# Performance work log

Hardware: AMD Instinct MI355X
Metric: run time of the kernel (lower is better)

## Reference

```python
import jax, jax.numpy as jnp
import numpy as np

P = 128        # num proposals
C_ALL = 19     # instance_classes + 1
C = 18         # instance classes used in the loop
M = 400000     # total (proposal, point) membership entries
N_PTS = 65536  # num points
SCORE_THR = 0.001
MASK_THR = -0.5
NPOINT_THR = 100


def setup_inputs() -> dict:
    key = jax.random.key(0)
    k1, k2, k3, k4, k5 = jax.random.split(key, 5)
    return {
        "cls_scores": jax.random.normal(k1, (P, C_ALL), dtype=jnp.float32),
        "scores": jax.random.normal(k2, (P, C_ALL), dtype=jnp.float32),
        "mask_scores": jax.random.normal(k3, (M, C_ALL), dtype=jnp.float32),
        "prop_ids": jax.random.randint(k4, (M,), 0, P, dtype=jnp.int32),
        "point_ids": jax.random.randint(k5, (M,), 0, N_PTS, dtype=jnp.int32),
        "num_points": N_PTS,
    }


def reference(cls_scores, scores, mask_scores, prop_ids, point_ids, num_points):
    # cls_scores, scores: [P, C+1]; mask_scores: [M, C+1]
    # prop_ids/point_ids: [M] -> membership of point in proposal
    n_prop = cls_scores.shape[0]
    cls_soft = jax.nn.softmax(cls_scores, axis=1)              # [P, C+1]
    # scores_pred_i = clamp(scores[:, i], 0, 1) * cls_soft[:, i], for each class i
    scores_pred = (jnp.clip(scores[:, :C], 0.0, 1.0) * cls_soft[:, :C]).T  # [C, P]

    # per-class mask threshold then scatter 1s into dense [P, N] proposal masks
    mask_keep = (mask_scores[:, :C] > MASK_THR).astype(jnp.int32).T        # [C, M]

    def scatter_one_class(m):
        # duplicates resolved with max (matches repeated assignment of 1)
        return jnp.zeros((n_prop, num_points), jnp.int32).at[prop_ids, point_ids].max(m)

    dense = jax.vmap(scatter_one_class)(mask_keep)             # [C, P, N] int32

    pointnum = dense.sum(axis=-1)                              # [C, P]
    keep = (cls_soft[:, :C].T > SCORE_THR) \
        & (scores_pred > -1.0) \
        & (pointnum >= NPOINT_THR)                             # [C, P]

    proposals_pred = dense * keep[..., None].astype(jnp.int32)  # zero invalid rows
    cluster_scores = jnp.where(keep, scores_pred, 0.0)
    semantic_id = jnp.broadcast_to((jnp.arange(C) + 1)[:, None], (C, n_prop))
    return proposals_pred, cluster_scores, keep, semantic_id
```

## Files before the change

### kernel.cpp

```cpp
#include <hip/hip_runtime.h>
#include <stdint.h>

#define NPROP   128
#define C_ALL   19
#define NCLS    18
#define M_TOTAL 400000
#define NPTS    65536
#define CP      (NCLS * NPROP)
#define PTS_PER_CHUNK 8192
#define NCHUNK  (NPTS / PTS_PER_CHUNK)

struct WS {
    float        spred[CP];
    unsigned int keepA[CP];
    unsigned int pointnum[CP];
    unsigned int dense[(size_t)NPROP * NPTS];
};

__global__ void zero_kernel(WS* ws) {
    const size_t tid = (size_t)blockIdx.x * blockDim.x + threadIdx.x;
    const size_t stride = (size_t)gridDim.x * blockDim.x;
    uint4* d4 = (uint4*)ws->dense;
    const size_t n4 = (size_t)NPROP * NPTS / 4;
    const uint4 z = make_uint4(0u, 0u, 0u, 0u);
    for (size_t j = tid; j < n4; j += stride) d4[j] = z;
    if (tid < CP) ws->pointnum[tid] = 0;
}

__global__ void prep_kernel(const float* __restrict__ cls_scores,
                            const float* __restrict__ scores,
                            WS* ws) {
    int p = threadIdx.x;
    if (p >= NPROP) return;
    float row[C_ALL];
    float mx = -3.4e38f;
    #pragma unroll
    for (int i = 0; i < C_ALL; ++i) {
        row[i] = cls_scores[p * C_ALL + i];
        mx = fmaxf(mx, row[i]);
    }
    float s = 0.0f;
    #pragma unroll
    for (int i = 0; i < C_ALL; ++i) {
        row[i] = __expf(row[i] - mx);
        s += row[i];
    }
    float inv = 1.0f / s;
    #pragma unroll
    for (int c = 0; c < NCLS; ++c) {
        float soft = row[c] * inv;
        float sc = scores[p * C_ALL + c];
        sc = fminf(fmaxf(sc, 0.0f), 1.0f);
        float sp = sc * soft;
        ws->spred[c * NPROP + p] = sp;
        ws->keepA[c * NPROP + p] = (soft > 0.001f && sp > -1.0f) ? 1u : 0u;
    }
}

__global__ void scatter_kernel(const float* __restrict__ mask_scores,
                               const int* __restrict__ prop_ids,
                               const int* __restrict__ point_ids,
                               WS* ws) {
    int m = blockIdx.x * blockDim.x + threadIdx.x;
    if (m >= M_TOTAL) return;
    const float* r = mask_scores + (size_t)m * C_ALL;
    unsigned int bits = 0;
    #pragma unroll
    for (int c = 0; c < NCLS; ++c)
        bits |= (unsigned int)(r[c] > -0.5f) << c;
    const size_t addr = ((size_t)prop_ids[m] << 16) | (unsigned int)point_ids[m];
    atomicOr(&ws->dense[addr], bits);
}

__global__ __launch_bounds__(256) void count_kernel(WS* ws) {
    __shared__ unsigned int cnt[NCLS];
    const int p = blockIdx.x;
    const int chunk = blockIdx.y;
    const int t = threadIdx.x;
    if (t < NCLS) cnt[t] = 0;
    __syncthreads();

    const unsigned int* base = ws->dense + ((size_t)p << 16) + chunk * (NPTS / 4);
    unsigned int local[NCLS] = {0};
    for (int i = t; i < NPTS / 4; i += 256) {
        unsigned int w = base[i];
        #pragma unroll
        for (int c = 0; c < NCLS; ++c) local[c] += (w >> c) & 1u;
    }
    #pragma unroll
    for (int c = 0; c < NCLS; ++c) {
        unsigned int v = local[c];
        #pragma unroll
        for (int off = 32; off > 0; off >>= 1) v += __shfl_down(v, off, 64);
        if ((t & 63) == 0) atomicAdd(&cnt[c], v);
    }
    __syncthreads();
    if (t < NCLS) atomicAdd(&ws->pointnum[t * NPROP + p], cnt[t]);
}

__global__ __launch_bounds__(256) void write_kernel(const WS* __restrict__ ws,
                                                    float* __restrict__ out) {
    __shared__ unsigned int lds[PTS_PER_CHUNK];
    __shared__ float sk[NCLS];
    const int p = blockIdx.x;
    const int chunk = blockIdx.y;
    const int t = threadIdx.x;

    const uint4* src4 = (const uint4*)(ws->dense + ((size_t)p << 16) + chunk * PTS_PER_CHUNK);
    uint4* lds4 = (uint4*)lds;
    #pragma unroll
    for (int j = 0; j < (PTS_PER_CHUNK / 4) / 256; ++j)
        lds4[j * 256 + t] = src4[j * 256 + t];

    if (t < NCLS) {
        const int cp = t * NPROP + p;
        const bool k = (ws->keepA[cp] != 0u) && (ws->pointnum[cp] >= 100u);
        sk[t] = k ? 1.0f : 0.0f;
        if (chunk == 0) {
            float* outCS = out + (size_t)CP * NPTS;
            float* outK  = outCS + CP;
            float* outS  = outK  + CP;
            outCS[cp] = k ? ws->spred[cp] : 0.0f;
            outK[cp]  = k ? 1.0f : 0.0f;
            outS[cp]  = (float)(t + 1);
        }
    }
    __syncthreads();

    const float4 z = make_float4(0.f, 0.f, 0.f, 0.f);
    #pragma unroll 1
    for (int c = 0; c < NCLS; ++c) {
        float4* dst = (float4*)(out + (((size_t)(c * NPROP + p)) << 16)) +
                      chunk * (PTS_PER_CHUNK / 4);
        if (sk[c] != 0.0f) {
            #pragma unroll
            for (int j = 0; j < (PTS_PER_CHUNK / 4) / 256; ++j) {
                const int idx = j * 256 + t;
                uint4 w = lds4[idx];
                float4 v;
                v.x = (w.x >> c) & 1u ? 1.0f : 0.0f;
                v.y = (w.y >> c) & 1u ? 1.0f : 0.0f;
                v.z = (w.z >> c) & 1u ? 1.0f : 0.0f;
                v.w = (w.w >> c) & 1u ? 1.0f : 0.0f;
                dst[idx] = v;
            }
        } else {
            #pragma unroll
            for (int j = 0; j < (PTS_PER_CHUNK / 4) / 256; ++j)
                dst[j * 256 + t] = z;
        }
    }
}

extern "C" void kernel_launch(void* const* d_in, const int* in_sizes, int n_in,
                              void* d_out, int out_size, void* d_ws, size_t ws_size,
                              hipStream_t stream) {
    const float* cls_scores  = (const float*)d_in[0];
    const float* scores      = (const float*)d_in[1];
    const float* mask_scores = (const float*)d_in[2];
    const int*   prop_ids    = (const int*)d_in[3];
    const int*   point_ids   = (const int*)d_in[4];

    WS* ws = (WS*)d_ws;
    float* out = (float*)d_out;

    zero_kernel<<<2048, 256, 0, stream>>>(ws);
    prep_kernel<<<1, NPROP, 0, stream>>>(cls_scores, scores, ws);

    const int blocksM = (M_TOTAL + 255) / 256;
    scatter_kernel<<<blocksM, 256, 0, stream>>>(mask_scores, prop_ids, point_ids, ws);

    count_kernel<<<dim3(NPROP, 4), 256, 0, stream>>>(ws);
    write_kernel<<<dim3(NPROP, NCHUNK), 256, 0, stream>>>(ws, out);
}
```

Baseline: 172.3 us.

## Fuse zero/prep kernels, vectorize count loads, nontemporal branchless output writes

Merges the workspace zeroing and softmax prep into one launch, removing one kernel launch. The count kernel now reads uint4 words with a fully unrolled loop. The write kernel swaps grid order so the chunk index is the fast dimension, replaces the keep branch with a multiply-select by the keep flag, and uses nontemporal stores for the large float output. The aim is lower launch overhead and better streaming-store throughput on the output, which is about 600 MB. The cost is that rows that are not kept now read LDS and do the bit tests too.

```diff
diff --git a/kernel.cpp b/kernel.cpp
--- a/kernel.cpp
+++ b/kernel.cpp
@@ -8,7 +8,9 @@
 #define NPTS    65536
 #define CP      (NCLS * NPROP)
 #define PTS_PER_CHUNK 8192
-#define NCHUNK  (NPTS / PTS_PER_CHUNK)
+#define NCHUNK  8
+
+typedef float f32x4 __attribute__((ext_vector_type(4)));
 
 struct WS {
     float        spred[CP];
@@ -17,7 +19,8 @@
     unsigned int dense[(size_t)NPROP * NPTS];
 };
 
-__global__ void zero_kernel(WS* ws) {
+__global__ void zero_prep_kernel(const float* __restrict__ cls_scores,
+                                 const float* __restrict__ scores, WS* ws) {
     const size_t tid = (size_t)blockIdx.x * blockDim.x + threadIdx.x;
     const size_t stride = (size_t)gridDim.x * blockDim.x;
     uint4* d4 = (uint4*)ws->dense;
@@ -25,35 +28,31 @@
     const uint4 z = make_uint4(0u, 0u, 0u, 0u);
     for (size_t j = tid; j < n4; j += stride) d4[j] = z;
     if (tid < CP) ws->pointnum[tid] = 0;
-}
-
-__global__ void prep_kernel(const float* __restrict__ cls_scores,
-                            const float* __restrict__ scores,
-                            WS* ws) {
-    int p = threadIdx.x;
-    if (p >= NPROP) return;
-    float row[C_ALL];
-    float mx = -3.4e38f;
-    #pragma unroll
-    for (int i = 0; i < C_ALL; ++i) {
-        row[i] = cls_scores[p * C_ALL + i];
-        mx = fmaxf(mx, row[i]);
-    }
-    float s = 0.0f;
-    #pragma unroll
-    for (int i = 0; i < C_ALL; ++i) {
-        row[i] = __expf(row[i] - mx);
-        s += row[i];
-    }
-    float inv = 1.0f / s;
-    #pragma unroll
-    for (int c = 0; c < NCLS; ++c) {
-        float soft = row[c] * inv;
-        float sc = scores[p * C_ALL + c];
-        sc = fminf(fmaxf(sc, 0.0f), 1.0f);
-        float sp = sc * soft;
-        ws->spred[c * NPROP + p] = sp;
-        ws->keepA[c * NPROP + p] = (soft > 0.001f && sp > -1.0f) ? 1u : 0u;
+    if (tid < NPROP) {
+        const int p = (int)tid;
+        float row[C_ALL];
+        float mx = -3.4e38f;
+        #pragma unroll
+        for (int i = 0; i < C_ALL; ++i) {
+            row[i] = cls_scores[p * C_ALL + i];
+            mx = fmaxf(mx, row[i]);
+        }
+        float s = 0.0f;
+        #pragma unroll
+        for (int i = 0; i < C_ALL; ++i) {
+            row[i] = __expf(row[i] - mx);
+            s += row[i];
+        }
+        const float inv = 1.0f / s;
+        #pragma unroll
+        for (int c = 0; c < NCLS; ++c) {
+            const float soft = row[c] * inv;
+            float sc = scores[p * C_ALL + c];
+            sc = fminf(fmaxf(sc, 0.0f), 1.0f);
+            const float sp = sc * soft;
+            ws->spred[c * NPROP + p] = sp;
+            ws->keepA[c * NPROP + p] = (soft > 0.001f && sp > -1.0f) ? 1u : 0u;
+        }
     }
 }
 
@@ -75,23 +74,28 @@
 __global__ __launch_bounds__(256) void count_kernel(WS* ws) {
     __shared__ unsigned int cnt[NCLS];
     const int p = blockIdx.x;
-    const int chunk = blockIdx.y;
+    const int quarter = blockIdx.y;
     const int t = threadIdx.x;
     if (t < NCLS) cnt[t] = 0;
     __syncthreads();
-
-    const unsigned int* base = ws->dense + ((size_t)p << 16) + chunk * (NPTS / 4);
-    unsigned int local[NCLS] = {0};
-    for (int i = t; i < NPTS / 4; i += 256) {
-        unsigned int w = base[i];
+    const uint4* base4 = (const uint4*)(ws->dense + ((size_t)p << 16) +
+                                        quarter * (NPTS / 4));
+    unsigned int local[NCLS];
+    #pragma unroll
+    for (int c = 0; c < NCLS; ++c) local[c] = 0;
+    #pragma unroll
+    for (int j = 0; j < (NPTS / 16) / 256; ++j) {
+        const uint4 w = base4[j * 256 + t];
         #pragma unroll
-        for (int c = 0; c < NCLS; ++c) local[c] += (w >> c) & 1u;
+        for (int c = 0; c < NCLS; ++c)
+            local[c] += ((w.x >> c) & 1u) + ((w.y >> c) & 1u) +
+                        ((w.z >> c) & 1u) + ((w.w >> c) & 1u);
     }
     #pragma unroll
     for (int c = 0; c < NCLS; ++c) {
         unsigned int v = local[c];
         #pragma unroll
-        for (int off = 32; off > 0; off >>= 1) v += __shfl_down(v, off, 64);
+        for (int off = 32; off; off >>= 1) v += __shfl_down(v, off, 64);
         if ((t & 63) == 0) atomicAdd(&cnt[c], v);
     }
     __syncthreads();
@@ -102,11 +106,12 @@
                                                     float* __restrict__ out) {
     __shared__ unsigned int lds[PTS_PER_CHUNK];
     __shared__ float sk[NCLS];
-    const int p = blockIdx.x;
-    const int chunk = blockIdx.y;
-    const int t = threadIdx.x;
+    const int chunk = blockIdx.x;
+    const int p     = blockIdx.y;
+    const int t     = threadIdx.x;
 
-    const uint4* src4 = (const uint4*)(ws->dense + ((size_t)p << 16) + chunk * PTS_PER_CHUNK);
+    const uint4* src4 = (const uint4*)(ws->dense + ((size_t)p << 16) +
+                                       chunk * PTS_PER_CHUNK);
     uint4* lds4 = (uint4*)lds;
     #pragma unroll
     for (int j = 0; j < (PTS_PER_CHUNK / 4) / 256; ++j)
@@ -127,27 +132,21 @@
     }
     __syncthreads();
 
-    const float4 z = make_float4(0.f, 0.f, 0.f, 0.f);
     #pragma unroll 1
     for (int c = 0; c < NCLS; ++c) {
-        float4* dst = (float4*)(out + (((size_t)(c * NPROP + p)) << 16)) +
-                      chunk * (PTS_PER_CHUNK / 4);
-        if (sk[c] != 0.0f) {
-            #pragma unroll
-            for (int j = 0; j < (PTS_PER_CHUNK / 4) / 256; ++j) {
-                const int idx = j * 256 + t;
-                uint4 w = lds4[idx];
-                float4 v;
-                v.x = (w.x >> c) & 1u ? 1.0f : 0.0f;
-                v.y = (w.y >> c) & 1u ? 1.0f : 0.0f;
-                v.z = (w.z >> c) & 1u ? 1.0f : 0.0f;
-                v.w = (w.w >> c) & 1u ? 1.0f : 0.0f;
-                dst[idx] = v;
-            }
-        } else {
-            #pragma unroll
-            for (int j = 0; j < (PTS_PER_CHUNK / 4) / 256; ++j)
-                dst[j * 256 + t] = z;
+        const float kf = sk[c];
+        f32x4* dst = (f32x4*)(out + (((size_t)(c * NPROP + p)) << 16)) +
+                     chunk * (PTS_PER_CHUNK / 4);
+        #pragma unroll
+        for (int j = 0; j < (PTS_PER_CHUNK / 4) / 256; ++j) {
+            const int idx = j * 256 + t;
+            const uint4 w = lds4[idx];
+            f32x4 v;
+            v.x = ((w.x >> c) & 1u) ? kf : 0.0f;
+            v.y = ((w.y >> c) & 1u) ? kf : 0.0f;
+            v.z = ((w.z >> c) & 1u) ? kf : 0.0f;
+            v.w = ((w.w >> c) & 1u) ? kf : 0.0f;
+            __builtin_nontemporal_store(v, &dst[idx]);
         }
     }
 }
@@ -164,12 +163,9 @@
     WS* ws = (WS*)d_ws;
     float* out = (float*)d_out;
 
-    zero_kernel<<<2048, 256, 0, stream>>>(ws);
-    prep_kernel<<<1, NPROP, 0, stream>>>(cls_scores, scores, ws);
-
+    zero_prep_kernel<<<2048, 256, 0, stream>>>(cls_scores, scores, ws);
     const int blocksM = (M_TOTAL + 255) / 256;
     scatter_kernel<<<blocksM, 256, 0, stream>>>(mask_scores, prop_ids, point_ids, ws);
-
     count_kernel<<<dim3(NPROP, 4), 256, 0, stream>>>(ws);
-    write_kernel<<<dim3(NPROP, NCHUNK), 256, 0, stream>>>(ws, out);
+    write_kernel<<<dim3(NCHUNK, NPROP), 256, 0, stream>>>(ws, out);
 }
```

Measured after the change: 177.9 us. +3.2%, slower.
